# Kernel tuning notes

Measured on AMD Instinct MI355X. Metric: run time of the kernel, lower is better.

The kernel has to match this reference:

```python
import jax, jax.numpy as jnp
import numpy as np

N = 100000
E = 3200000
IN_DIM = 512
OUT_DIM = 128


def setup_inputs() -> dict:
    key = jax.random.key(0)
    k1, k2, k3 = jax.random.split(key, 3)
    x = jax.random.normal(k1, (N, IN_DIM), dtype=jnp.float32)
    edge_index = jax.random.randint(k2, (2, E), 0, N, dtype=jnp.int64)
    # Glorot init like PyG GCNConv
    W = jax.random.normal(k3, (IN_DIM, OUT_DIM), dtype=jnp.float32) * (2.0 / (IN_DIM + OUT_DIM)) ** 0.5
    b = jnp.zeros((OUT_DIM,), dtype=jnp.float32)
    return {"x": x, "edge_index": edge_index, "W": W, "b": b}


def gcn_conv(x, edge_index, W, b):
    # GCNConv with add_self_loops=True, normalize=True (symmetric norm)
    row, col = edge_index[0], edge_index[1]  # messages flow row -> col
    xw = x @ W  # [N, out_dim]
    ones = jnp.ones((E,), dtype=xw.dtype)
    # degree of destination nodes, +1 for self-loop
    deg = jax.ops.segment_sum(ones, col, num_segments=N) + 1.0
    dinv = jax.lax.rsqrt(deg)  # deg^{-1/2}, deg >= 1 so no inf
    norm = dinv[row] * dinv[col]  # [E]
    msg = xw[row] * norm[:, None]  # gather + scale
    out = jax.ops.segment_sum(msg, col, num_segments=N)  # scatter-add
    # self-loop contribution: norm_ii = dinv_i * dinv_i
    out = out + xw * (dinv * dinv)[:, None]
    return out + b


def reference(x, edge_index, W, b):
    return gcn_conv(x, edge_index, W, b)
```

## Files before the change

kernel.cpp:

```cpp
#include <hip/hip_runtime.h>
#include <hip/hip_bf16.h>

using short8  = __attribute__((ext_vector_type(8))) short;
using f32x4   = __attribute__((ext_vector_type(4))) float;
using uint32x4 = __attribute__((ext_vector_type(4))) unsigned;

static constexpr int N_NODES = 100000;
static constexpr int N_EDGES = 3200000;
static constexpr int IN_DIM  = 512;
static constexpr int OUT_DIM = 128;
static constexpr int NBINS   = (N_NODES + 255) / 256;
static constexpr int NB      = 1024;
static constexpr int CHUNK   = N_EDGES / NB;
static constexpr int EPB     = (CHUNK + 255) / 256;
static constexpr int SLACK   = 9216;
static constexpr int RSH     = 13;
static constexpr int NRANGE  = (N_NODES + (1 << RSH) - 1) >> RSH;

__device__ __forceinline__ short f2bf(float f) {
  unsigned u = __builtin_bit_cast(unsigned, f);
  u = (u + 0x7FFFu + ((u >> 16) & 1u)) >> 16;
  return (short)u;
}

__device__ __forceinline__ void gload16(const void* g, void* l) {
  __builtin_amdgcn_global_load_lds(
      (const __attribute__((address_space(1))) unsigned int*)g,
      (__attribute__((address_space(3))) unsigned int*)l, 16, 0, 0);
}

__global__ __launch_bounds__(256) void cast_WT(const float* __restrict__ W,
                                               short* __restrict__ WT,
                                               int* __restrict__ cursor) {
  const int idx = blockIdx.x * 256 + threadIdx.x;
  if (idx < NBINS) cursor[idx] = idx * SLACK;
  const int c = idx >> 9, k = idx & 511;
  WT[(size_t)c * 512 + k] = f2bf(W[(size_t)k * 128 + c]);
}

__global__ __launch_bounds__(256) void gemm_lds(const float* __restrict__ x,
                                                const short* __restrict__ WT,
                                                const float* __restrict__ dinv,
                                                unsigned short* __restrict__ xwb) {
  __shared__ float          Abuf[2][128 * 32];
  __shared__ unsigned short Bbuf[2][128 * 32];
  const int tid = threadIdx.x;
  const int w   = tid >> 6;
  const int l   = tid & 63;
  const int wr  = w >> 1, wc = w & 1;
  const int lr  = l & 15;
  const int lk  = l >> 4;
  const int row0 = blockIdx.x * 128;
  const char* xb  = reinterpret_cast<const char*>(x);
  const char* wtb = reinterpret_cast<const char*>(WT);
  const int wbase = (tid & ~63) * 16;

  auto stage = [&](int kb, int buf) {
#pragma unroll
    for (int t = 0; t < 4; ++t) {
      const int f = t * 256 + tid;
      const int r = f >> 3;
      const int u = f & 7;
      const int grow = min(row0 + r, N_NODES - 1);
      const char* src = xb + (size_t)grow * 2048 + kb * 128 + ((u ^ (r & 7)) << 4);
      gload16(src, (char*)Abuf[buf] + t * 4096 + wbase);
    }
#pragma unroll
    for (int t = 0; t < 2; ++t) {
      const int f = t * 256 + tid;
      const int c = f >> 2;
      const int u = f & 3;
      const char* src = wtb + (size_t)c * 1024 + kb * 64 + ((u ^ (c & 3)) << 4);
      gload16(src, (char*)Bbuf[buf] + t * 4096 + wbase);
    }
  };

  auto cvt2 = [](float lo, float hi) -> unsigned {
    __hip_bfloat162 h = __float22bfloat162_rn(make_float2(lo, hi));
    unsigned r;
    __builtin_memcpy(&r, &h, 4);
    return r;
  };

  f32x4 acc[4][4] = {};

  auto compute = [&](int buf) {
    const char* Ab = (const char*)Abuf[buf];
    const char* Bb = (const char*)Bbuf[buf];
    short8 a[4], b[4];
#pragma unroll
    for (int rf = 0; rf < 4; ++rf) {
      const int rl = wr * 64 + rf * 16 + lr;
      const char* base = Ab + rl * 128;
      const f32x4 r0 = *(const f32x4*)(base + (((2 * lk)     ^ (rl & 7)) << 4));
      const f32x4 r1 = *(const f32x4*)(base + (((2 * lk + 1) ^ (rl & 7)) << 4));
      uint32x4 ua;
      ua[0] = cvt2(r0[0], r0[1]);
      ua[1] = cvt2(r0[2], r0[3]);
      ua[2] = cvt2(r1[0], r1[1]);
      ua[3] = cvt2(r1[2], r1[3]);
      a[rf] = __builtin_bit_cast(short8, ua);
    }
#pragma unroll
    for (int cf = 0; cf < 4; ++cf) {
      const int cl = wc * 64 + cf * 16 + lr;
      b[cf] = *(const short8*)(Bb + cl * 64 + ((lk ^ (cl & 3)) << 4));
    }
#pragma unroll
    for (int rf = 0; rf < 4; ++rf)
#pragma unroll
      for (int cf = 0; cf < 4; ++cf)
        acc[rf][cf] = __builtin_amdgcn_mfma_f32_16x16x32_bf16(a[rf], b[cf], acc[rf][cf], 0, 0, 0);
  };

  stage(0, 0);
  __syncthreads();
  for (int kb = 0; kb < 16; ++kb) {
    if (kb < 15) stage(kb + 1, (kb + 1) & 1);
    compute(kb & 1);
    __syncthreads();
  }

#pragma unroll
  for (int rf = 0; rf < 4; ++rf) {
#pragma unroll
    for (int j = 0; j < 4; ++j) {
      const int row = row0 + wr * 64 + rf * 16 + lk * 4 + j;
      if (row < N_NODES) {
        const float sc = dinv[row];
        unsigned short* o = &xwb[(size_t)row * OUT_DIM + wc * 64 + lr];
#pragma unroll
        for (int cf = 0; cf < 4; ++cf)
          o[cf * 16] = (unsigned short)f2bf(acc[rf][cf][j] * sc);
      }
    }
  }
}

__global__ __launch_bounds__(256) void bin_scatter(const int* __restrict__ erow,
                                                   const int* __restrict__ ecol,
                                                   int* __restrict__ cursor,
                                                   unsigned* __restrict__ benc) {
  __shared__ int hist[NBINS];
  __shared__ int cur[NBINS];
  const int blk = blockIdx.x, tid = threadIdx.x;
  const int e0 = blk * CHUNK;
  for (int i = tid; i < NBINS; i += 256) hist[i] = 0;
  __syncthreads();

  int cc[EPB], rr[EPB];
#pragma unroll
  for (int i = 0; i < EPB; ++i) {
    const int e = e0 + tid + i * 256;
    const bool ok = (tid + i * 256) < CHUNK;
    cc[i] = ok ? ecol[e] : -1;
    rr[i] = ok ? erow[e] : 0;
    if (ok) atomicAdd(&hist[cc[i] >> 8], 1);
  }
  __syncthreads();
  for (int i = tid; i < NBINS; i += 256)
    cur[i] = hist[i] ? atomicAdd(&cursor[i], hist[i]) : 0;
  __syncthreads();
#pragma unroll
  for (int i = 0; i < EPB; ++i) {
    if (cc[i] >= 0) {
      const unsigned enc = (unsigned)rr[i] | ((unsigned)(cc[i] & 255) << 24);
      const int p = atomicAdd(&cur[cc[i] >> 8], 1);
      benc[p] = enc;
    }
  }
}

__global__ __launch_bounds__(256) void bin_build(const unsigned* __restrict__ benc,
                                                 const int* __restrict__ cursor,
                                                 int* __restrict__ brow,
                                                 int* __restrict__ offs,
                                                 int* __restrict__ oend,
                                                 float* __restrict__ dinv) {
  __shared__ int hist[256 * NRANGE];
  __shared__ int sh[256];
  const int b = blockIdx.x, tid = threadIdx.x;
  const int e0 = b * SLACK;
  const int e1 = cursor[b];
  for (int i = tid; i < 256 * NRANGE; i += 256) hist[i] = 0;
  __syncthreads();
  for (int e = e0 + tid; e < e1; e += 256) {
    const unsigned v = benc[e];
    const int key = (int)(v >> 24) * NRANGE + (int)((v & 0x00FFFFFFu) >> RSH);
    atomicAdd(&hist[key], 1);
  }
  __syncthreads();
  const int base = tid * NRANGE;
  int d0 = 0;
#pragma unroll
  for (int r = 0; r < NRANGE; ++r) {
    const int c = hist[base + r];
    hist[base + r] = d0;
    d0 += c;
  }
  sh[tid] = d0;
  __syncthreads();
  for (int d = 1; d < 256; d <<= 1) {
    const int tv = (tid >= d) ? sh[tid - d] : 0;
    __syncthreads();
    sh[tid] += tv;
    __syncthreads();
  }
  const int myoff = e0 + sh[tid] - d0;
#pragma unroll
  for (int r = 0; r < NRANGE; ++r) hist[base + r] += myoff;
  const int node = (b << 8) + tid;
  if (node < N_NODES) {
    offs[node] = myoff;
    oend[node] = myoff + d0;
    dinv[node] = rsqrtf((float)d0 + 1.0f);
  }
  __syncthreads();
  for (int e = e0 + tid; e < e1; e += 256) {
    const unsigned v = benc[e];
    const int src = (int)(v & 0x00FFFFFFu);
    const int key = (int)(v >> 24) * NRANGE + (src >> RSH);
    const int p = atomicAdd(&hist[key], 1);
    brow[p] = src;
  }
}

__global__ __launch_bounds__(256) void gather_out(const unsigned short* __restrict__ xwb,
                                                  const float* __restrict__ dinv,
                                                  const int* __restrict__ offs,
                                                  const int* __restrict__ oend,
                                                  const int* __restrict__ brow,
                                                  const float* __restrict__ bias,
                                                  float* __restrict__ out) {
  const int lane = threadIdx.x & 63;
  const int node = blockIdx.x * (blockDim.x >> 6) + (threadIdx.x >> 6);
  if (node >= N_NODES) return;
  const float di = dinv[node];
  const int c0 = lane * 2;

  auto ld2 = [&](int r) -> float2 {
    const unsigned v = *reinterpret_cast<const unsigned*>(&xwb[(size_t)r * OUT_DIM + c0]);
    float2 f;
    f.x = __builtin_bit_cast(float, v << 16);
    f.y = __builtin_bit_cast(float, v & 0xFFFF0000u);
    return f;
  };

  float2 acc = ld2(node);
  float2 acc2 = make_float2(0.f, 0.f);

  int e = offs[node];
  const int e1 = oend[node];
  for (; e + 16 <= e1; e += 16) {
    int r[16];
#pragma unroll
    for (int i = 0; i < 16; ++i) r[i] = brow[e + i];
    float2 v[16];
#pragma unroll
    for (int i = 0; i < 16; ++i) v[i] = ld2(r[i]);
#pragma unroll
    for (int i = 0; i < 16; i += 2) {
      acc.x += v[i].x + v[i + 1].x;
      acc.y += v[i].y + v[i + 1].y;
    }
  }
  for (; e + 4 <= e1; e += 4) {
    const int r0 = brow[e], r1 = brow[e + 1], r2 = brow[e + 2], r3 = brow[e + 3];
    const float2 v0 = ld2(r0), v1 = ld2(r1), v2 = ld2(r2), v3 = ld2(r3);
    acc2.x += (v0.x + v1.x) + (v2.x + v3.x);
    acc2.y += (v0.y + v1.y) + (v2.y + v3.y);
  }
  for (; e < e1; ++e) {
    const float2 v = ld2(brow[e]);
    acc2.x += v.x;
    acc2.y += v.y;
  }
  acc.x += acc2.x;
  acc.y += acc2.y;

  const float2 bb = *reinterpret_cast<const float2*>(&bias[c0]);
  float2 o;
  o.x = acc.x * di + bb.x;
  o.y = acc.y * di + bb.y;
  *reinterpret_cast<float2*>(&out[(size_t)node * OUT_DIM + c0]) = o;
}

extern "C" void kernel_launch(void* const* d_in, const int* in_sizes, int n_in,
                              void* d_out, int out_size, void* d_ws, size_t ws_size,
                              hipStream_t stream) {
  const float* x    = (const float*)d_in[0];
  const int*   eidx = (const int*)d_in[1];
  const float* W    = (const float*)d_in[2];
  const float* b    = (const float*)d_in[3];
  float* out = (float*)d_out;

  const int* erow = eidx;
  const int* ecol = eidx + N_EDGES;

  char* ws = (char*)d_ws;
  size_t off = 0;
  auto alloc = [&](size_t bytes) -> void* {
    void* p = ws + off;
    off = (off + bytes + 255) & ~(size_t)255;
    return p;
  };
  unsigned short* xwb = (unsigned short*)alloc((size_t)N_NODES * OUT_DIM * sizeof(short));
  short* WT      = (short*)alloc((size_t)OUT_DIM * IN_DIM * sizeof(short));
  float* dinv    = (float*)alloc((size_t)N_NODES * sizeof(float));
  int*   offs    = (int*)alloc((size_t)N_NODES * sizeof(int));
  int*   oend    = (int*)alloc((size_t)N_NODES * sizeof(int));
  int*   cursor  = (int*)alloc((size_t)NBINS * sizeof(int));
  int*   brow    = (int*)alloc((size_t)NBINS * SLACK * sizeof(int));
  unsigned* benc = (unsigned*)alloc((size_t)NBINS * SLACK * sizeof(unsigned));

  cast_WT<<<256, 256, 0, stream>>>(W, WT, cursor);
  bin_scatter<<<NB, 256, 0, stream>>>(erow, ecol, cursor, benc);
  bin_build<<<NBINS, 256, 0, stream>>>(benc, cursor, brow, offs, oend, dinv);
  gemm_lds<<<(N_NODES + 127) / 128, 256, 0, stream>>>(x, WT, dinv, xwb);
  gather_out<<<(N_NODES + 3) / 4, 256, 0, stream>>>(xwb, dinv, offs, oend, brow, b, out);
}
```

Baseline: 262.9 us.

## Process gather source-range by range across 16 nodes per wave for cache locality

bin_build now stores per-node, per-source-range offsets (NRANGE+1 arrays) rather than just start/end. gather_out gives each wave 16 destination nodes and walks the source ranges in an outer loop, so concurrent gathers hit a narrower window of xwb rows and reuse L2/MALL better. The cost is less memory-level parallelism per wave (2-wide unroll instead of 16), more offset loads and branches, and a grid with 16x fewer waves, which may cut occupancy and latency hiding.

```diff
diff --git a/kernel.cpp b/kernel.cpp
--- a/kernel.cpp
+++ b/kernel.cpp
@@ -174,8 +174,7 @@
 __global__ __launch_bounds__(256) void bin_build(const unsigned* __restrict__ benc,
                                                  const int* __restrict__ cursor,
                                                  int* __restrict__ brow,
-                                                 int* __restrict__ offs,
-                                                 int* __restrict__ oend,
+                                                 int* __restrict__ offs2,
                                                  float* __restrict__ dinv) {
   __shared__ int hist[256 * NRANGE];
   __shared__ int sh[256];
@@ -207,12 +206,14 @@
     __syncthreads();
   }
   const int myoff = e0 + sh[tid] - d0;
-#pragma unroll
-  for (int r = 0; r < NRANGE; ++r) hist[base + r] += myoff;
   const int node = (b << 8) + tid;
+#pragma unroll
+  for (int r = 0; r < NRANGE; ++r) {
+    hist[base + r] += myoff;
+    if (node < N_NODES) offs2[(size_t)r * N_NODES + node] = hist[base + r];
+  }
   if (node < N_NODES) {
-    offs[node] = myoff;
-    oend[node] = myoff + d0;
+    offs2[(size_t)NRANGE * N_NODES + node] = myoff + d0;
     dinv[node] = rsqrtf((float)d0 + 1.0f);
   }
   __syncthreads();
@@ -227,16 +228,14 @@
 
 __global__ __launch_bounds__(256) void gather_out(const unsigned short* __restrict__ xwb,
                                                   const float* __restrict__ dinv,
-                                                  const int* __restrict__ offs,
-                                                  const int* __restrict__ oend,
+                                                  const int* __restrict__ offs2,
                                                   const int* __restrict__ brow,
                                                   const float* __restrict__ bias,
                                                   float* __restrict__ out) {
-  const int lane = threadIdx.x & 63;
-  const int node = blockIdx.x * (blockDim.x >> 6) + (threadIdx.x >> 6);
-  if (node >= N_NODES) return;
-  const float di = dinv[node];
-  const int c0 = lane * 2;
+  const int lane  = threadIdx.x & 63;
+  const int wv    = threadIdx.x >> 6;
+  const int nbase = blockIdx.x * 64 + wv * 16;
+  const int c0    = lane * 2;
 
   auto ld2 = [&](int r) -> float2 {
     const unsigned v = *reinterpret_cast<const unsigned*>(&xwb[(size_t)r * OUT_DIM + c0]);
@@ -246,43 +245,47 @@
     return f;
   };
 
-  float2 acc = ld2(node);
-  float2 acc2 = make_float2(0.f, 0.f);
-
-  int e = offs[node];
-  const int e1 = oend[node];
-  for (; e + 16 <= e1; e += 16) {
-    int r[16];
-#pragma unroll
-    for (int i = 0; i < 16; ++i) r[i] = brow[e + i];
-    float2 v[16];
-#pragma unroll
-    for (int i = 0; i < 16; ++i) v[i] = ld2(r[i]);
-#pragma unroll
-    for (int i = 0; i < 16; i += 2) {
-      acc.x += v[i].x + v[i + 1].x;
-      acc.y += v[i].y + v[i + 1].y;
-    }
-  }
-  for (; e + 4 <= e1; e += 4) {
-    const int r0 = brow[e], r1 = brow[e + 1], r2 = brow[e + 2], r3 = brow[e + 3];
-    const float2 v0 = ld2(r0), v1 = ld2(r1), v2 = ld2(r2), v3 = ld2(r3);
-    acc2.x += (v0.x + v1.x) + (v2.x + v3.x);
-    acc2.y += (v0.y + v1.y) + (v2.y + v3.y);
-  }
-  for (; e < e1; ++e) {
-    const float2 v = ld2(brow[e]);
-    acc2.x += v.x;
-    acc2.y += v.y;
-  }
-  acc.x += acc2.x;
-  acc.y += acc2.y;
+  float2 acc[16];
+#pragma unroll
+  for (int i = 0; i < 16; ++i) {
+    const int node = nbase + i;
+    acc[i] = (node < N_NODES) ? ld2(node) : make_float2(0.f, 0.f);
+  }
+
+  for (int r = 0; r < NRANGE; ++r) {
+    const int* ob = offs2 + (size_t)r * N_NODES;
+#pragma unroll
+    for (int i = 0; i < 16; ++i) {
+      const int node = nbase + i;
+      if (node >= N_NODES) continue;
+      int e = ob[node];
+      const int e1 = ob[N_NODES + node];
+      for (; e + 2 <= e1; e += 2) {
+        const int r0 = brow[e], r1 = brow[e + 1];
+        const float2 v0 = ld2(r0), v1 = ld2(r1);
+        acc[i].x += v0.x + v1.x;
+        acc[i].y += v0.y + v1.y;
+      }
+      if (e < e1) {
+        const float2 v = ld2(brow[e]);
+        acc[i].x += v.x;
+        acc[i].y += v.y;
+      }
+    }
+  }
 
   const float2 bb = *reinterpret_cast<const float2*>(&bias[c0]);
-  float2 o;
-  o.x = acc.x * di + bb.x;
-  o.y = acc.y * di + bb.y;
-  *reinterpret_cast<float2*>(&out[(size_t)node * OUT_DIM + c0]) = o;
+#pragma unroll
+  for (int i = 0; i < 16; ++i) {
+    const int node = nbase + i;
+    if (node < N_NODES) {
+      const float di = dinv[node];
+      float2 o;
+      o.x = acc[i].x * di + bb.x;
+      o.y = acc[i].y * di + bb.y;
+      *reinterpret_cast<float2*>(&out[(size_t)node * OUT_DIM + c0]) = o;
+    }
+  }
 }
 
 extern "C" void kernel_launch(void* const* d_in, const int* in_sizes, int n_in,
@@ -307,15 +310,14 @@
   unsigned short* xwb = (unsigned short*)alloc((size_t)N_NODES * OUT_DIM * sizeof(short));
   short* WT      = (short*)alloc((size_t)OUT_DIM * IN_DIM * sizeof(short));
   float* dinv    = (float*)alloc((size_t)N_NODES * sizeof(float));
-  int*   offs    = (int*)alloc((size_t)N_NODES * sizeof(int));
-  int*   oend    = (int*)alloc((size_t)N_NODES * sizeof(int));
+  int*   offs2   = (int*)alloc((size_t)(NRANGE + 1) * N_NODES * sizeof(int));
   int*   cursor  = (int*)alloc((size_t)NBINS * sizeof(int));
   int*   brow    = (int*)alloc((size_t)NBINS * SLACK * sizeof(int));
   unsigned* benc = (unsigned*)alloc((size_t)NBINS * SLACK * sizeof(unsigned));
 
   cast_WT<<<256, 256, 0, stream>>>(W, WT, cursor);
   bin_scatter<<<NB, 256, 0, stream>>>(erow, ecol, cursor, benc);
-  bin_build<<<NBINS, 256, 0, stream>>>(benc, cursor, brow, offs, oend, dinv);
+  bin_build<<<NBINS, 256, 0, stream>>>(benc, cursor, brow, offs2, dinv);
   gemm_lds<<<(N_NODES + 127) / 128, 256, 0, stream>>>(x, WT, dinv, xwb);
-  gather_out<<<(N_NODES + 3) / 4, 256, 0, stream>>>(xwb, dinv, offs, oend, brow, b, out);
-}
+  gather_out<<<(N_NODES + 63) / 64, 256, 0, stream>>>(xwb, dinv, offs2, brow, b, out);
+}
```

Result: slower. 606.1 us (+130.6%).
